# Performance work log

Hardware: AMD Instinct MI355X
Metric: run time of the kernel (lower is better)

## Reference

```python
import jax, jax.numpy as jnp
import numpy as np

EPS = 0.0  # GIN epsilon (train_eps=False)

def setup_inputs() -> dict:
    key = jax.random.key(0)
    k_x, k_e, k_w1, k_w2 = jax.random.split(key, 4)
    N, E, D = 100000, 625000, 128
    x = jax.random.normal(k_x, (N, D), dtype=jnp.float32)
    edge_index = jax.random.randint(k_e, (2, E), 0, N, dtype=jnp.int32)
    s = 1.0 / np.sqrt(D)
    W1 = jax.random.normal(k_w1, (D, D), dtype=jnp.float32) * s
    b1 = jnp.zeros((D,), dtype=jnp.float32)
    W2 = jax.random.normal(k_w2, (D, D), dtype=jnp.float32) * s
    b2 = jnp.zeros((D,), dtype=jnp.float32)
    return {"x": x, "edge_index": edge_index, "W1": W1, "b1": b1, "W2": W2, "b2": b2}

def reference(x, edge_index, W1, b1, W2, b2):
    # GINConv: out_i = MLP((1+eps)*x_i + sum_{j in N(i)} x_j)
    src = edge_index[0]
    dst = edge_index[1]
    agg = jax.ops.segment_sum(x[src], dst, num_segments=x.shape[0])  # [N, D]
    h = (1.0 + EPS) * x + agg
    # MLP: Linear -> ReLU -> Dropout(eval: identity) -> Linear
    h = jax.nn.relu(h @ W1.T + b1)
    h = h @ W2.T + b2
    # outer activation; outer dropout is identity in eval
    return jax.nn.relu(h)
```

## Files before the change

### kernel.cpp

```cpp
#include <hip/hip_runtime.h>


#define D 128
#define HLD 136
#define CPIT 40
#define KSLOT 32
#define CSTR 32

typedef __attribute__((ext_vector_type(8))) short bf16x8;
typedef __attribute__((ext_vector_type(4))) float f32x4;

__device__ __forceinline__ short f2bf(float f) {
    union { float f; unsigned u; } v; v.f = f;
    unsigned r = v.u + 0x7fffu + ((v.u >> 16) & 1u);
    return (short)(r >> 16);
}
__device__ __forceinline__ float bflo(unsigned u) {
    union { unsigned u; float f; } v; v.u = u << 16; return v.f;
}
__device__ __forceinline__ float bfhi(unsigned u) {
    union { unsigned u; float f; } v; v.u = u & 0xffff0000u; return v.f;
}
__device__ __forceinline__ unsigned pack2(float a, float b) {
    return ((unsigned)(unsigned short)f2bf(a)) | (((unsigned)(unsigned short)f2bf(b)) << 16);
}

__global__ __launch_bounds__(256) void convert_fill(const float4* __restrict__ x4,
                                                    unsigned short* __restrict__ xb,
                                                    const int* __restrict__ ei,
                                                    int* __restrict__ cnt,
                                                    int* __restrict__ bucket,
                                                    int nConv, int nFillBlocks, int E) {
    if ((int)blockIdx.x < nFillBlocks) {
        int t8 = blockIdx.x * 256 + threadIdx.x;
        int E8 = E >> 3;
        if (t8 < E8) {
            const int4* ei4 = (const int4*)ei;
            int E4 = E >> 2;
            int4 s0 = ei4[2 * t8],      s1 = ei4[2 * t8 + 1];
            int4 d0 = ei4[E4 + 2 * t8], d1 = ei4[E4 + 2 * t8 + 1];
            int sl;
            sl = atomicAdd(&cnt[d0.x * CSTR], 1); if (sl < KSLOT) bucket[d0.x * KSLOT + sl] = s0.x;
            sl = atomicAdd(&cnt[d0.y * CSTR], 1); if (sl < KSLOT) bucket[d0.y * KSLOT + sl] = s0.y;
            sl = atomicAdd(&cnt[d0.z * CSTR], 1); if (sl < KSLOT) bucket[d0.z * KSLOT + sl] = s0.z;
            sl = atomicAdd(&cnt[d0.w * CSTR], 1); if (sl < KSLOT) bucket[d0.w * KSLOT + sl] = s0.w;
            sl = atomicAdd(&cnt[d1.x * CSTR], 1); if (sl < KSLOT) bucket[d1.x * KSLOT + sl] = s1.x;
            sl = atomicAdd(&cnt[d1.y * CSTR], 1); if (sl < KSLOT) bucket[d1.y * KSLOT + sl] = s1.y;
            sl = atomicAdd(&cnt[d1.z * CSTR], 1); if (sl < KSLOT) bucket[d1.z * KSLOT + sl] = s1.z;
            sl = atomicAdd(&cnt[d1.w * CSTR], 1); if (sl < KSLOT) bucket[d1.w * KSLOT + sl] = s1.w;
        }
    } else {
        int t = ((int)blockIdx.x - nFillBlocks) * 256 + threadIdx.x;
        if (t < nConv) {
            float4 a = x4[2 * t], b = x4[2 * t + 1];
            bf16x8 r;
            r[0] = f2bf(a.x); r[1] = f2bf(a.y); r[2] = f2bf(a.z); r[3] = f2bf(a.w);
            r[4] = f2bf(b.x); r[5] = f2bf(b.y); r[6] = f2bf(b.z); r[7] = f2bf(b.w);
            ((bf16x8*)xb)[t] = r;
        }
    }
}

__global__ __launch_bounds__(256) void gather_kernel(const uint4* __restrict__ xb4,
                                                     const int* __restrict__ cnt,
                                                     const int* __restrict__ bucket,
                                                     uint4* __restrict__ h04, int N) {
    int g = blockIdx.x * 256 + threadIdx.x;
    int node = g >> 4;
    if (node >= N) return;
    int lane = g & 15;
    int deg = cnt[node * CSTR];
    deg = deg < KSLOT ? deg : KSLOT;
    const int bb = node * KSLOT;

    uint4 sv = xb4[node * 16 + lane];
    float a0 = bflo(sv.x), a1 = bfhi(sv.x), a2 = bflo(sv.y), a3 = bfhi(sv.y);
    float a4 = bflo(sv.z), a5 = bfhi(sv.z), a6 = bflo(sv.w), a7 = bfhi(sv.w);

    int e = 0;
    for (; e + 3 < deg; e += 4) {
        int s0 = bucket[bb + e], s1 = bucket[bb + e + 1];
        int s2 = bucket[bb + e + 2], s3 = bucket[bb + e + 3];
        uint4 p0 = xb4[s0 * 16 + lane];
        uint4 p1 = xb4[s1 * 16 + lane];
        uint4 p2 = xb4[s2 * 16 + lane];
        uint4 p3 = xb4[s3 * 16 + lane];
        a0 += bflo(p0.x) + bflo(p1.x) + bflo(p2.x) + bflo(p3.x);
        a1 += bfhi(p0.x) + bfhi(p1.x) + bfhi(p2.x) + bfhi(p3.x);
        a2 += bflo(p0.y) + bflo(p1.y) + bflo(p2.y) + bflo(p3.y);
        a3 += bfhi(p0.y) + bfhi(p1.y) + bfhi(p2.y) + bfhi(p3.y);
        a4 += bflo(p0.z) + bflo(p1.z) + bflo(p2.z) + bflo(p3.z);
        a5 += bfhi(p0.z) + bfhi(p1.z) + bfhi(p2.z) + bfhi(p3.z);
        a6 += bflo(p0.w) + bflo(p1.w) + bflo(p2.w) + bflo(p3.w);
        a7 += bfhi(p0.w) + bfhi(p1.w) + bfhi(p2.w) + bfhi(p3.w);
    }
    for (; e < deg; ++e) {
        uint4 p = xb4[bucket[bb + e] * 16 + lane];
        a0 += bflo(p.x); a1 += bfhi(p.x); a2 += bflo(p.y); a3 += bfhi(p.y);
        a4 += bflo(p.z); a5 += bfhi(p.z); a6 += bflo(p.w); a7 += bfhi(p.w);
    }
    uint4 r;
    r.x = pack2(a0, a1);
    r.y = pack2(a2, a3);
    r.z = pack2(a4, a5);
    r.w = pack2(a6, a7);
    h04[node * 16 + lane] = r;
}

__global__ __launch_bounds__(512, 4) void mlp_fused(const short* __restrict__ h0,
                                                    const float* __restrict__ W1,
                                                    const float* __restrict__ b1,
                                                    const float* __restrict__ W2,
                                                    const float* __restrict__ b2,
                                                    float* __restrict__ out, int N) {
    __shared__ short W1l[D * HLD];
    __shared__ short W2l[D * HLD];
    __shared__ short chunk[8 * 16 * CPIT];

    {
        const float4* W14 = (const float4*)W1;
        const float4* W24 = (const float4*)W2;
        for (int idx = threadIdx.x; idx < D * (D / 4); idx += 512) {
            int n = idx >> 5;
            int k4 = idx & 31;
            float4 w = W14[idx];
            short* dp = &W1l[n * HLD + k4 * 4];
            dp[0] = f2bf(w.x); dp[1] = f2bf(w.y); dp[2] = f2bf(w.z); dp[3] = f2bf(w.w);
            w = W24[idx];
            dp = &W2l[n * HLD + k4 * 4];
            dp[0] = f2bf(w.x); dp[1] = f2bf(w.y); dp[2] = f2bf(w.z); dp[3] = f2bf(w.w);
        }
    }
    __syncthreads();

    const int wave = threadIdx.x >> 6;
    const int lane = threadIdx.x & 63;
    const int m = lane & 15;
    const int quad = lane >> 4;
    const int tiles = (N + 127) / 128;
    short* ch = &chunk[wave * 16 * CPIT];

    float b1r[8], b2r[8];
#pragma unroll
    for (int j = 0; j < 8; ++j) { b1r[j] = b1[j * 16 + m]; b2r[j] = b2[j * 16 + m]; }

    for (int t = blockIdx.x; t < tiles; t += gridDim.x) {
        const int r0 = t * 128 + wave * 16;
        const int arow = r0 + m;

        bf16x8 afrag[4];
        if (arow < N) {
#pragma unroll
            for (int ks = 0; ks < 4; ++ks)
                afrag[ks] = *(const bf16x8*)&h0[(long long)arow * D + ks * 32 + quad * 8];
        } else {
#pragma unroll
            for (int ks = 0; ks < 4; ++ks) afrag[ks] = (bf16x8)(short)0;
        }

        f32x4 acc2[8];
#pragma unroll
        for (int jt = 0; jt < 8; ++jt) acc2[jt] = (f32x4)0.0f;

#pragma unroll
        for (int ks2 = 0; ks2 < 4; ++ks2) {
            f32x4 acc1[2];
            acc1[0] = (f32x4)0.0f;
            acc1[1] = (f32x4)0.0f;
#pragma unroll
            for (int half = 0; half < 2; ++half) {
                int jt = 2 * ks2 + half;
#pragma unroll
                for (int ks = 0; ks < 4; ++ks) {
                    bf16x8 b = *(const bf16x8*)&W1l[(jt * 16 + m) * HLD + ks * 32 + quad * 8];
                    acc1[half] = __builtin_amdgcn_mfma_f32_16x16x32_bf16(afrag[ks], b, acc1[half], 0, 0, 0);
                }
            }
#pragma unroll
            for (int half = 0; half < 2; ++half) {
                float bv = b1r[2 * ks2 + half];
#pragma unroll
                for (int i = 0; i < 4; ++i) {
                    float v = acc1[half][i] + bv;
                    v = v > 0.0f ? v : 0.0f;
                    ch[(quad * 4 + i) * CPIT + half * 16 + m] = f2bf(v);
                }
            }
            bf16x8 a2 = *(const bf16x8*)&ch[m * CPIT + quad * 8];
#pragma unroll
            for (int jt2 = 0; jt2 < 8; ++jt2) {
                bf16x8 b = *(const bf16x8*)&W2l[(jt2 * 16 + m) * HLD + ks2 * 32 + quad * 8];
                acc2[jt2] = __builtin_amdgcn_mfma_f32_16x16x32_bf16(a2, b, acc2[jt2], 0, 0, 0);
            }
        }

#pragma unroll
        for (int jt2 = 0; jt2 < 8; ++jt2) {
            int col = jt2 * 16 + m;
            float bv = b2r[jt2];
#pragma unroll
            for (int i = 0; i < 4; ++i) {
                int row = r0 + quad * 4 + i;
                if (row < N) {
                    float v = acc2[jt2][i] + bv;
                    v = v > 0.0f ? v : 0.0f;
                    __builtin_nontemporal_store(v, &out[(long long)row * D + col]);
                }
            }
        }
    }
}

extern "C" void kernel_launch(void* const* d_in, const int* in_sizes, int n_in,
                              void* d_out, int out_size, void* d_ws, size_t ws_size,
                              hipStream_t stream) {
    const float* x  = (const float*)d_in[0];
    const int*   ei = (const int*)d_in[1];
    const float* W1 = (const float*)d_in[2];
    const float* b1 = (const float*)d_in[3];
    const float* W2 = (const float*)d_in[4];
    const float* b2 = (const float*)d_in[5];
    float* out = (float*)d_out;

    const int N = in_sizes[0] / D;
    const int E = in_sizes[1] / 2;

    unsigned short* h0 = (unsigned short*)d_ws;
    unsigned short* xb = h0 + (size_t)N * D;
    int* cnt    = (int*)(xb + (size_t)N * D);
    int* bucket = cnt + (size_t)N * CSTR;

    hipMemsetAsync(cnt, 0, (size_t)N * CSTR * sizeof(int), stream);

    {
        int nConv = N * (D / 8);
        int nConvBlocks = (nConv + 255) / 256;
        int nFillBlocks = ((E >> 3) + 255) / 256;
        convert_fill<<<nFillBlocks + nConvBlocks, 256, 0, stream>>>(
            (const float4*)x, xb, ei, cnt, bucket, nConv, nFillBlocks, E);
    }

    {
        long long thr = (long long)N * 16;
        gather_kernel<<<(int)((thr + 255) / 256), 256, 0, stream>>>(
            (const uint4*)xb, cnt, bucket, (uint4*)h0, N);
    }

    mlp_fused<<<512, 512, 0, stream>>>((const short*)h0, W1, b1, W2, b2, out, N);
}
```

Before: 193.0 us.

## Fuse all GIN stages into one cooperative persistent kernel with grid syncs

Replaces the memset plus three kernel launches with a single cooperative kernel. It zeroes the counters, fills the edge buckets and converts x to bf16, gathers neighbours, then runs the fused MLP, with grid-wide syncs between phases. Weights are staged into LDS once per block at the start. This removes launch and inter-kernel gaps, but the grid is capped at 512 blocks for every phase and each grid.sync adds a barrier. The atomic-heavy fill phase also gets only a fixed fraction of blocks, so the memory-bound phases may lose parallelism.

```diff
diff --git a/kernel.cpp b/kernel.cpp
--- a/kernel.cpp
+++ b/kernel.cpp
@@ -1,4 +1,7 @@
 #include <hip/hip_runtime.h>
+#include <hip/hip_cooperative_groups.h>
+
+namespace cg = cooperative_groups;
 
 
 #define D 128
@@ -24,6 +27,233 @@
 __device__ __forceinline__ unsigned pack2(float a, float b) {
     return ((unsigned)(unsigned short)f2bf(a)) | (((unsigned)(unsigned short)f2bf(b)) << 16);
 }
+
+
+__device__ __forceinline__ void fill_edges8(const int4* __restrict__ ei4, int E4,
+                                            int* __restrict__ cnt, int* __restrict__ bucket,
+                                            int t8) {
+    int4 s0 = ei4[2 * t8],      s1 = ei4[2 * t8 + 1];
+    int4 d0 = ei4[E4 + 2 * t8], d1 = ei4[E4 + 2 * t8 + 1];
+    int sl;
+    sl = atomicAdd(&cnt[d0.x * CSTR], 1); if (sl < KSLOT) bucket[d0.x * KSLOT + sl] = s0.x;
+    sl = atomicAdd(&cnt[d0.y * CSTR], 1); if (sl < KSLOT) bucket[d0.y * KSLOT + sl] = s0.y;
+    sl = atomicAdd(&cnt[d0.z * CSTR], 1); if (sl < KSLOT) bucket[d0.z * KSLOT + sl] = s0.z;
+    sl = atomicAdd(&cnt[d0.w * CSTR], 1); if (sl < KSLOT) bucket[d0.w * KSLOT + sl] = s0.w;
+    sl = atomicAdd(&cnt[d1.x * CSTR], 1); if (sl < KSLOT) bucket[d1.x * KSLOT + sl] = s1.x;
+    sl = atomicAdd(&cnt[d1.y * CSTR], 1); if (sl < KSLOT) bucket[d1.y * KSLOT + sl] = s1.y;
+    sl = atomicAdd(&cnt[d1.z * CSTR], 1); if (sl < KSLOT) bucket[d1.z * KSLOT + sl] = s1.z;
+    sl = atomicAdd(&cnt[d1.w * CSTR], 1); if (sl < KSLOT) bucket[d1.w * KSLOT + sl] = s1.w;
+}
+
+__device__ __forceinline__ void convert8(const float4* __restrict__ x4,
+                                         unsigned short* __restrict__ xb, int t) {
+    float4 a = x4[2 * t], b = x4[2 * t + 1];
+    bf16x8 r;
+    r[0] = f2bf(a.x); r[1] = f2bf(a.y); r[2] = f2bf(a.z); r[3] = f2bf(a.w);
+    r[4] = f2bf(b.x); r[5] = f2bf(b.y); r[6] = f2bf(b.z); r[7] = f2bf(b.w);
+    ((bf16x8*)xb)[t] = r;
+}
+
+__device__ __forceinline__ void gather_node16(const uint4* __restrict__ xb4,
+                                              const int* __restrict__ cnt,
+                                              const int* __restrict__ bucket,
+                                              uint4* __restrict__ h04,
+                                              int node, int lane16) {
+    int deg = cnt[node * CSTR];
+    deg = deg < KSLOT ? deg : KSLOT;
+    const int bb = node * KSLOT;
+    uint4 sv = xb4[node * 16 + lane16];
+    float a0 = bflo(sv.x), a1 = bfhi(sv.x), a2 = bflo(sv.y), a3 = bfhi(sv.y);
+    float a4 = bflo(sv.z), a5 = bfhi(sv.z), a6 = bflo(sv.w), a7 = bfhi(sv.w);
+    int e = 0;
+    for (; e + 3 < deg; e += 4) {
+        int s0 = bucket[bb + e], s1 = bucket[bb + e + 1];
+        int s2 = bucket[bb + e + 2], s3 = bucket[bb + e + 3];
+        uint4 p0 = xb4[s0 * 16 + lane16];
+        uint4 p1 = xb4[s1 * 16 + lane16];
+        uint4 p2 = xb4[s2 * 16 + lane16];
+        uint4 p3 = xb4[s3 * 16 + lane16];
+        a0 += bflo(p0.x) + bflo(p1.x) + bflo(p2.x) + bflo(p3.x);
+        a1 += bfhi(p0.x) + bfhi(p1.x) + bfhi(p2.x) + bfhi(p3.x);
+        a2 += bflo(p0.y) + bflo(p1.y) + bflo(p2.y) + bflo(p3.y);
+        a3 += bfhi(p0.y) + bfhi(p1.y) + bfhi(p2.y) + bfhi(p3.y);
+        a4 += bflo(p0.z) + bflo(p1.z) + bflo(p2.z) + bflo(p3.z);
+        a5 += bfhi(p0.z) + bfhi(p1.z) + bfhi(p2.z) + bfhi(p3.z);
+        a6 += bflo(p0.w) + bflo(p1.w) + bflo(p2.w) + bflo(p3.w);
+        a7 += bfhi(p0.w) + bfhi(p1.w) + bfhi(p2.w) + bfhi(p3.w);
+    }
+    for (; e < deg; ++e) {
+        uint4 p = xb4[bucket[bb + e] * 16 + lane16];
+        a0 += bflo(p.x); a1 += bfhi(p.x); a2 += bflo(p.y); a3 += bfhi(p.y);
+        a4 += bflo(p.z); a5 += bfhi(p.z); a6 += bflo(p.w); a7 += bfhi(p.w);
+    }
+    uint4 r;
+    r.x = pack2(a0, a1);
+    r.y = pack2(a2, a3);
+    r.z = pack2(a4, a5);
+    r.w = pack2(a6, a7);
+    h04[node * 16 + lane16] = r;
+}
+
+__device__ __forceinline__ void mlp_tile(const short* __restrict__ h0s,
+                                         const short* __restrict__ W1l,
+                                         const short* __restrict__ W2l,
+                                         short* __restrict__ ch,
+                                         const float* b1r, const float* b2r,
+                                         float* __restrict__ out,
+                                         int t, int wave, int m, int quad, int N) {
+    const int r0 = t * 128 + wave * 16;
+    const int arow = r0 + m;
+
+    bf16x8 afrag[4];
+    if (arow < N) {
+#pragma unroll
+        for (int ks = 0; ks < 4; ++ks)
+            afrag[ks] = *(const bf16x8*)&h0s[(long long)arow * D + ks * 32 + quad * 8];
+    } else {
+#pragma unroll
+        for (int ks = 0; ks < 4; ++ks) afrag[ks] = (bf16x8)(short)0;
+    }
+
+    f32x4 acc2[8];
+#pragma unroll
+    for (int jt = 0; jt < 8; ++jt) acc2[jt] = (f32x4)0.0f;
+
+#pragma unroll
+    for (int ks2 = 0; ks2 < 4; ++ks2) {
+        f32x4 acc1[2];
+        acc1[0] = (f32x4)0.0f;
+        acc1[1] = (f32x4)0.0f;
+#pragma unroll
+        for (int half = 0; half < 2; ++half) {
+            int jt = 2 * ks2 + half;
+#pragma unroll
+            for (int ks = 0; ks < 4; ++ks) {
+                bf16x8 b = *(const bf16x8*)&W1l[(jt * 16 + m) * HLD + ks * 32 + quad * 8];
+                acc1[half] = __builtin_amdgcn_mfma_f32_16x16x32_bf16(afrag[ks], b, acc1[half], 0, 0, 0);
+            }
+        }
+#pragma unroll
+        for (int half = 0; half < 2; ++half) {
+            float bv = b1r[2 * ks2 + half];
+#pragma unroll
+            for (int i = 0; i < 4; ++i) {
+                float v = acc1[half][i] + bv;
+                v = v > 0.0f ? v : 0.0f;
+                ch[(quad * 4 + i) * CPIT + half * 16 + m] = f2bf(v);
+            }
+        }
+        bf16x8 a2 = *(const bf16x8*)&ch[m * CPIT + quad * 8];
+#pragma unroll
+        for (int jt2 = 0; jt2 < 8; ++jt2) {
+            bf16x8 b = *(const bf16x8*)&W2l[(jt2 * 16 + m) * HLD + ks2 * 32 + quad * 8];
+            acc2[jt2] = __builtin_amdgcn_mfma_f32_16x16x32_bf16(a2, b, acc2[jt2], 0, 0, 0);
+        }
+    }
+
+#pragma unroll
+    for (int jt2 = 0; jt2 < 8; ++jt2) {
+        int col = jt2 * 16 + m;
+        float bv = b2r[jt2];
+#pragma unroll
+        for (int i = 0; i < 4; ++i) {
+            int row = t * 128 + wave * 16 + quad * 4 + i;
+            if (row < N) {
+                float v = acc2[jt2][i] + bv;
+                v = v > 0.0f ? v : 0.0f;
+                __builtin_nontemporal_store(v, &out[(long long)row * D + col]);
+            }
+        }
+    }
+}
+
+__device__ __forceinline__ void stage_weights(const float* __restrict__ W1,
+                                              const float* __restrict__ W2,
+                                              short* __restrict__ W1l,
+                                              short* __restrict__ W2l,
+                                              int tid, int nthr) {
+    const float4* W14 = (const float4*)W1;
+    const float4* W24 = (const float4*)W2;
+    for (int idx = tid; idx < D * (D / 4); idx += nthr) {
+        int n = idx >> 5;
+        int k4 = idx & 31;
+        float4 w = W14[idx];
+        short* dp = &W1l[n * HLD + k4 * 4];
+        dp[0] = f2bf(w.x); dp[1] = f2bf(w.y); dp[2] = f2bf(w.z); dp[3] = f2bf(w.w);
+        w = W24[idx];
+        dp = &W2l[n * HLD + k4 * 4];
+        dp[0] = f2bf(w.x); dp[1] = f2bf(w.y); dp[2] = f2bf(w.z); dp[3] = f2bf(w.w);
+    }
+}
+
+__global__ __launch_bounds__(512) void gin_mega(
+    const float4* __restrict__ x4, unsigned short* __restrict__ xb,
+    const int* __restrict__ ei, int* __restrict__ cnt, int* __restrict__ bucket,
+    unsigned short* __restrict__ h0,
+    const float* __restrict__ W1, const float* __restrict__ b1,
+    const float* __restrict__ W2, const float* __restrict__ b2,
+    float* __restrict__ out, int N, int E) {
+
+    __shared__ short W1l[D * HLD];
+    __shared__ short W2l[D * HLD];
+    __shared__ short chunk[8 * 16 * CPIT];
+
+    cg::grid_group grid = cg::this_grid();
+    const int tid = threadIdx.x;
+    const int nb = gridDim.x;
+
+    stage_weights(W1, W2, W1l, W2l, tid, 512);
+
+    {
+        int4* c4 = (int4*)cnt;
+        int total = (N * CSTR) >> 2;
+        int4 z; z.x = 0; z.y = 0; z.z = 0; z.w = 0;
+        for (int i = blockIdx.x * 512 + tid; i < total; i += nb * 512) c4[i] = z;
+    }
+    grid.sync();
+
+    {
+        int fillB = (nb * 3) >> 3;
+        if (fillB < 1) fillB = 1;
+        if ((int)blockIdx.x < fillB) {
+            const int4* ei4 = (const int4*)ei;
+            int E8 = E >> 3, E4 = E >> 2;
+            for (int t8 = blockIdx.x * 512 + tid; t8 < E8; t8 += fillB * 512)
+                fill_edges8(ei4, E4, cnt, bucket, t8);
+        } else {
+            int nConv = N * (D / 8);
+            for (int t = ((int)blockIdx.x - fillB) * 512 + tid; t < nConv;
+                 t += (nb - fillB) * 512)
+                convert8(x4, xb, t);
+        }
+    }
+    grid.sync();
+
+    {
+        const uint4* xb4 = (const uint4*)xb;
+        uint4* h04 = (uint4*)h0;
+        long long tasks = (long long)N * 16;
+        for (long long g = (long long)blockIdx.x * 512 + tid; g < tasks;
+             g += (long long)nb * 512)
+            gather_node16(xb4, cnt, bucket, h04, (int)(g >> 4), (int)(g & 15));
+    }
+    grid.sync();
+
+    {
+        const int wave = tid >> 6;
+        const int lane = tid & 63;
+        const int m = lane & 15;
+        const int quad = lane >> 4;
+        const int tiles = (N + 127) / 128;
+        short* ch = &chunk[wave * 16 * CPIT];
+        float b1r[8], b2r[8];
+#pragma unroll
+        for (int j = 0; j < 8; ++j) { b1r[j] = b1[j * 16 + m]; b2r[j] = b2[j * 16 + m]; }
+        for (int t = blockIdx.x; t < tiles; t += nb)
+            mlp_tile((const short*)h0, W1l, W2l, ch, b1r, b2r, out, t, wave, m, quad, N);
+    }
+}
+
 
 __global__ __launch_bounds__(256) void convert_fill(const float4* __restrict__ x4,
                                                     unsigned short* __restrict__ xb,
@@ -33,31 +263,10 @@
                                                     int nConv, int nFillBlocks, int E) {
     if ((int)blockIdx.x < nFillBlocks) {
         int t8 = blockIdx.x * 256 + threadIdx.x;
-        int E8 = E >> 3;
-        if (t8 < E8) {
-            const int4* ei4 = (const int4*)ei;
-            int E4 = E >> 2;
-            int4 s0 = ei4[2 * t8],      s1 = ei4[2 * t8 + 1];
-            int4 d0 = ei4[E4 + 2 * t8], d1 = ei4[E4 + 2 * t8 + 1];
-            int sl;
-            sl = atomicAdd(&cnt[d0.x * CSTR], 1); if (sl < KSLOT) bucket[d0.x * KSLOT + sl] = s0.x;
-            sl = atomicAdd(&cnt[d0.y * CSTR], 1); if (sl < KSLOT) bucket[d0.y * KSLOT + sl] = s0.y;
-            sl = atomicAdd(&cnt[d0.z * CSTR], 1); if (sl < KSLOT) bucket[d0.z * KSLOT + sl] = s0.z;
-            sl = atomicAdd(&cnt[d0.w * CSTR], 1); if (sl < KSLOT) bucket[d0.w * KSLOT + sl] = s0.w;
-            sl = atomicAdd(&cnt[d1.x * CSTR], 1); if (sl < KSLOT) bucket[d1.x * KSLOT + sl] = s1.x;
-            sl = atomicAdd(&cnt[d1.y * CSTR], 1); if (sl < KSLOT) bucket[d1.y * KSLOT + sl] = s1.y;
-            sl = atomicAdd(&cnt[d1.z * CSTR], 1); if (sl < KSLOT) bucket[d1.z * KSLOT + sl] = s1.z;
-            sl = atomicAdd(&cnt[d1.w * CSTR], 1); if (sl < KSLOT) bucket[d1.w * KSLOT + sl] = s1.w;
-        }
+        if (t8 < (E >> 3)) fill_edges8((const int4*)ei, E >> 2, cnt, bucket, t8);
     } else {
         int t = ((int)blockIdx.x - nFillBlocks) * 256 + threadIdx.x;
-        if (t < nConv) {
-            float4 a = x4[2 * t], b = x4[2 * t + 1];
-            bf16x8 r;
-            r[0] = f2bf(a.x); r[1] = f2bf(a.y); r[2] = f2bf(a.z); r[3] = f2bf(a.w);
-            r[4] = f2bf(b.x); r[5] = f2bf(b.y); r[6] = f2bf(b.z); r[7] = f2bf(b.w);
-            ((bf16x8*)xb)[t] = r;
-        }
+        if (t < nConv) convert8(x4, xb, t);
     }
 }
 
@@ -68,43 +277,7 @@
     int g = blockIdx.x * 256 + threadIdx.x;
     int node = g >> 4;
     if (node >= N) return;
-    int lane = g & 15;
-    int deg = cnt[node * CSTR];
-    deg = deg < KSLOT ? deg : KSLOT;
-    const int bb = node * KSLOT;
-
-    uint4 sv = xb4[node * 16 + lane];
-    float a0 = bflo(sv.x), a1 = bfhi(sv.x), a2 = bflo(sv.y), a3 = bfhi(sv.y);
-    float a4 = bflo(sv.z), a5 = bfhi(sv.z), a6 = bflo(sv.w), a7 = bfhi(sv.w);
-
-    int e = 0;
-    for (; e + 3 < deg; e += 4) {
-        int s0 = bucket[bb + e], s1 = bucket[bb + e + 1];
-        int s2 = bucket[bb + e + 2], s3 = bucket[bb + e + 3];
-        uint4 p0 = xb4[s0 * 16 + lane];
-        uint4 p1 = xb4[s1 * 16 + lane];
-        uint4 p2 = xb4[s2 * 16 + lane];
-        uint4 p3 = xb4[s3 * 16 + lane];
-        a0 += bflo(p0.x) + bflo(p1.x) + bflo(p2.x) + bflo(p3.x);
-        a1 += bfhi(p0.x) + bfhi(p1.x) + bfhi(p2.x) + bfhi(p3.x);
-        a2 += bflo(p0.y) + bflo(p1.y) + bflo(p2.y) + bflo(p3.y);
-        a3 += bfhi(p0.y) + bfhi(p1.y) + bfhi(p2.y) + bfhi(p3.y);
-        a4 += bflo(p0.z) + bflo(p1.z) + bflo(p2.z) + bflo(p3.z);
-        a5 += bfhi(p0.z) + bfhi(p1.z) + bfhi(p2.z) + bfhi(p3.z);
-        a6 += bflo(p0.w) + bflo(p1.w) + bflo(p2.w) + bflo(p3.w);
-        a7 += bfhi(p0.w) + bfhi(p1.w) + bfhi(p2.w) + bfhi(p3.w);
-    }
-    for (; e < deg; ++e) {
-        uint4 p = xb4[bucket[bb + e] * 16 + lane];
-        a0 += bflo(p.x); a1 += bfhi(p.x); a2 += bflo(p.y); a3 += bfhi(p.y);
-        a4 += bflo(p.z); a5 += bfhi(p.z); a6 += bflo(p.w); a7 += bfhi(p.w);
-    }
-    uint4 r;
-    r.x = pack2(a0, a1);
-    r.y = pack2(a2, a3);
-    r.z = pack2(a4, a5);
-    r.w = pack2(a6, a7);
-    h04[node * 16 + lane] = r;
+    gather_node16(xb4, cnt, bucket, h04, node, g & 15);
 }
 
 __global__ __launch_bounds__(512, 4) void mlp_fused(const short* __restrict__ h0,
@@ -117,20 +290,7 @@
     __shared__ short W2l[D * HLD];
     __shared__ short chunk[8 * 16 * CPIT];
 
-    {
-        const float4* W14 = (const float4*)W1;
-        const float4* W24 = (const float4*)W2;
-        for (int idx = threadIdx.x; idx < D * (D / 4); idx += 512) {
-            int n = idx >> 5;
-            int k4 = idx & 31;
-            float4 w = W14[idx];
-            short* dp = &W1l[n * HLD + k4 * 4];
-            dp[0] = f2bf(w.x); dp[1] = f2bf(w.y); dp[2] = f2bf(w.z); dp[3] = f2bf(w.w);
-            w = W24[idx];
-            dp = &W2l[n * HLD + k4 * 4];
-            dp[0] = f2bf(w.x); dp[1] = f2bf(w.y); dp[2] = f2bf(w.z); dp[3] = f2bf(w.w);
-        }
-    }
+    stage_weights(W1, W2, W1l, W2l, threadIdx.x, 512);
     __syncthreads();
 
     const int wave = threadIdx.x >> 6;
@@ -144,71 +304,8 @@
 #pragma unroll
     for (int j = 0; j < 8; ++j) { b1r[j] = b1[j * 16 + m]; b2r[j] = b2[j * 16 + m]; }
 
-    for (int t = blockIdx.x; t < tiles; t += gridDim.x) {
-        const int r0 = t * 128 + wave * 16;
-        const int arow = r0 + m;
-
-        bf16x8 afrag[4];
-        if (arow < N) {
-#pragma unroll
-            for (int ks = 0; ks < 4; ++ks)
-                afrag[ks] = *(const bf16x8*)&h0[(long long)arow * D + ks * 32 + quad * 8];
-        } else {
-#pragma unroll
-            for (int ks = 0; ks < 4; ++ks) afrag[ks] = (bf16x8)(short)0;
-        }
-
-        f32x4 acc2[8];
-#pragma unroll
-        for (int jt = 0; jt < 8; ++jt) acc2[jt] = (f32x4)0.0f;
-
-#pragma unroll
-        for (int ks2 = 0; ks2 < 4; ++ks2) {
-            f32x4 acc1[2];
-            acc1[0] = (f32x4)0.0f;
-            acc1[1] = (f32x4)0.0f;
-#pragma unroll
-            for (int half = 0; half < 2; ++half) {
-                int jt = 2 * ks2 + half;
-#pragma unroll
-                for (int ks = 0; ks < 4; ++ks) {
-                    bf16x8 b = *(const bf16x8*)&W1l[(jt * 16 + m) * HLD + ks * 32 + quad * 8];
-                    acc1[half] = __builtin_amdgcn_mfma_f32_16x16x32_bf16(afrag[ks], b, acc1[half], 0, 0, 0);
-                }
-            }
-#pragma unroll
-            for (int half = 0; half < 2; ++half) {
-                float bv = b1r[2 * ks2 + half];
-#pragma unroll
-                for (int i = 0; i < 4; ++i) {
-                    float v = acc1[half][i] + bv;
-                    v = v > 0.0f ? v : 0.0f;
-                    ch[(quad * 4 + i) * CPIT + half * 16 + m] = f2bf(v);
-                }
-            }
-            bf16x8 a2 = *(const bf16x8*)&ch[m * CPIT + quad * 8];
-#pragma unroll
-            for (int jt2 = 0; jt2 < 8; ++jt2) {
-                bf16x8 b = *(const bf16x8*)&W2l[(jt2 * 16 + m) * HLD + ks2 * 32 + quad * 8];
-                acc2[jt2] = __builtin_amdgcn_mfma_f32_16x16x32_bf16(a2, b, acc2[jt2], 0, 0, 0);
-            }
-        }
-
-#pragma unroll
-        for (int jt2 = 0; jt2 < 8; ++jt2) {
-            int col = jt2 * 16 + m;
-            float bv = b2r[jt2];
-#pragma unroll
-            for (int i = 0; i < 4; ++i) {
-                int row = r0 + quad * 4 + i;
-                if (row < N) {
-                    float v = acc2[jt2][i] + bv;
-                    v = v > 0.0f ? v : 0.0f;
-                    __builtin_nontemporal_store(v, &out[(long long)row * D + col]);
-                }
-            }
-        }
-    }
+    for (int t = blockIdx.x; t < tiles; t += gridDim.x)
+        mlp_tile(h0, W1l, W2l, ch, b1r, b2r, out, t, wave, m, quad, N);
 }
 
 extern "C" void kernel_launch(void* const* d_in, const int* in_sizes, int n_in,
@@ -222,29 +319,40 @@
     const float* b2 = (const float*)d_in[5];
     float* out = (float*)d_out;
 
-    const int N = in_sizes[0] / D;
-    const int E = in_sizes[1] / 2;
+    int N = in_sizes[0] / D;
+    int E = in_sizes[1] / 2;
 
     unsigned short* h0 = (unsigned short*)d_ws;
     unsigned short* xb = h0 + (size_t)N * D;
     int* cnt    = (int*)(xb + (size_t)N * D);
     int* bucket = cnt + (size_t)N * CSTR;
 
-    hipMemsetAsync(cnt, 0, (size_t)N * CSTR * sizeof(int), stream);
-
-    {
+    bool done = false;
+    {
+        int maxB = 0;
+        hipError_t qe = hipOccupancyMaxActiveBlocksPerMultiprocessor(&maxB, gin_mega, 512, 0);
+        if (qe == hipSuccess && maxB > 0) {
+            int grid = maxB * 256;
+            if (grid > 512) grid = 512;
+            void* args[] = {(void*)&x, (void*)&xb, (void*)&ei, (void*)&cnt, (void*)&bucket,
+                            (void*)&h0, (void*)&W1, (void*)&b1, (void*)&W2, (void*)&b2,
+                            (void*)&out, (void*)&N, (void*)&E};
+            hipError_t le = hipLaunchCooperativeKernel((void*)gin_mega, dim3(grid),
+                                                       dim3(512), args, 0, stream);
+            done = (le == hipSuccess);
+        }
+    }
+
+    if (!done) {
+        hipMemsetAsync(cnt, 0, (size_t)N * CSTR * sizeof(int), stream);
         int nConv = N * (D / 8);
         int nConvBlocks = (nConv + 255) / 256;
         int nFillBlocks = ((E >> 3) + 255) / 256;
         convert_fill<<<nFillBlocks + nConvBlocks, 256, 0, stream>>>(
             (const float4*)x, xb, ei, cnt, bucket, nConv, nFillBlocks, E);
-    }
-
-    {
         long long thr = (long long)N * 16;
         gather_kernel<<<(int)((thr + 255) / 256), 256, 0, stream>>>(
             (const uint4*)xb, cnt, bucket, (uint4*)h0, N);
-    }
-
-    mlp_fused<<<512, 512, 0, stream>>>((const short*)h0, W1, b1, W2, b2, out, N);
-}
+        mlp_fused<<<512, 512, 0, stream>>>((const short*)h0, W1, b1, W2, b2, out, N);
+    }
+}
```

Measured after the change: 195.4 us. Within noise of the previous version (+1.2%).
